# Performance work log

Hardware: AMD Instinct MI355X
Metric: run time of the kernel (lower is better)

Reference implementation:

```python
import jax, jax.numpy as jnp
import numpy as np

B, S, D = 2, 2048, 1024
HQ, HKV = 16, 4
HD = D // HQ          # 64
DKV = HKV * HD        # 256
G = HQ // HKV         # 4 kv groups
SCALE = HD ** -0.5


def setup_inputs() -> dict:
    key = jax.random.key(0)
    ks = jax.random.split(key, 9)
    s = 0.02
    return {
        "q": jax.random.normal(ks[0], (B, S, D), dtype=jnp.float32),
        "Wq": jax.random.normal(ks[1], (D, D), dtype=jnp.float32) * s,
        "bq": jnp.zeros((D,), dtype=jnp.float32),
        "Wk": jax.random.normal(ks[2], (D, DKV), dtype=jnp.float32) * s,
        "bk": jnp.zeros((DKV,), dtype=jnp.float32),
        "Wv": jax.random.normal(ks[3], (D, DKV), dtype=jnp.float32) * s,
        "bv": jnp.zeros((DKV,), dtype=jnp.float32),
        "Wo": jax.random.normal(ks[4], (D, D), dtype=jnp.float32) * s,
        "bo": jnp.zeros((D,), dtype=jnp.float32),
    }


def reference(q, Wq, bq, Wk, bk, Wv, bv, Wo, bo):
    # self-attention: k = v = q (module defaults)
    qp = q @ Wq + bq                       # [B,S,D]
    kp = q @ Wk + bk                       # [B,S,DKV]
    vp = q @ Wv + bv                       # [B,S,DKV]
    qh = qp.reshape(B, S, HQ, HD).transpose(0, 2, 1, 3)    # [B,HQ,S,HD]
    kh = kp.reshape(B, S, HKV, HD)
    vh = vp.reshape(B, S, HKV, HD)
    # repeat_interleave kv heads along head dim (each kv head serves G q-heads)
    kh = jnp.repeat(kh, G, axis=2).transpose(0, 2, 1, 3)   # [B,HQ,S,HD]
    vh = jnp.repeat(vh, G, axis=2).transpose(0, 2, 1, 3)   # [B,HQ,S,HD]
    scores = jnp.einsum("bhqd,bhkd->bhqk", qh, kh) * SCALE  # [B,HQ,S,S]
    attn = jax.nn.softmax(scores, axis=-1)
    out = jnp.einsum("bhqk,bhkd->bhqd", attn, vh)           # [B,HQ,S,HD]
    out = out.transpose(0, 2, 1, 3).reshape(B, S, D)
    out = out @ Wo + bo
    return out, attn
```

## Files before the change

kernel.cpp:

```cpp
#include <hip/hip_runtime.h>
#include <stdint.h>

#define B_ 2
#define S_ 2048
#define D_ 1024
#define HD_ 64
#define DKV_ 256

typedef __attribute__((ext_vector_type(8))) __bf16 bf16x8;
typedef __attribute__((ext_vector_type(4))) float f32x4;
typedef __attribute__((ext_vector_type(4))) float float4v;
typedef __attribute__((ext_vector_type(4))) short s16x4;

__device__ __forceinline__ unsigned short f2bf(float f) {
  union { float f; uint32_t u; } v; v.f = f;
  uint32_t r = v.u + 0x7FFFu + ((v.u >> 16) & 1u);
  return (unsigned short)(r >> 16);
}

__device__ __forceinline__ void gload16(const void* g, void* l) {
  __builtin_amdgcn_global_load_lds(
      (const __attribute__((address_space(1))) uint32_t*)g,
      (__attribute__((address_space(3))) uint32_t*)l, 16, 0, 0);
}

__device__ __forceinline__ f32x4 mfma16(bf16x8 a, bf16x8 b, f32x4 c) {
  return __builtin_amdgcn_mfma_f32_16x16x32_bf16(a, b, c, 0, 0, 0);
}

__global__ void k_cvt(const float* __restrict__ in, unsigned short* __restrict__ out) {
  size_t i = ((size_t)blockIdx.x * 256 + threadIdx.x) * 4;
  float4v f = *(const float4v*)(in + i);
  s16x4 o;
#pragma unroll
  for (int r = 0; r < 4; ++r) o[r] = (short)f2bf(f[r]);
  *(s16x4*)(out + i) = o;
}

__global__ void k_tcvt_all(const float* __restrict__ Wq, const float* __restrict__ Wk,
                           const float* __restrict__ Wv, const float* __restrict__ Wo,
                           unsigned short* __restrict__ WqT, unsigned short* __restrict__ WkT,
                           unsigned short* __restrict__ WvT, unsigned short* __restrict__ WoT) {
  __shared__ unsigned short t[32][33];
  const int x = blockIdx.x;
  const float* W;
  unsigned short* Wt;
  int N, n0;
  if (x < 32)      { W = Wq; Wt = WqT; N = 1024; n0 = x * 32; }
  else if (x < 40) { W = Wk; Wt = WkT; N = 256;  n0 = (x - 32) * 32; }
  else if (x < 48) { W = Wv; Wt = WvT; N = 256;  n0 = (x - 40) * 32; }
  else             { W = Wo; Wt = WoT; N = 1024; n0 = (x - 48) * 32; }
  const int K = 1024, k0 = blockIdx.y * 32;
  int tx = threadIdx.x & 31, ty = threadIdx.x >> 5;
#pragma unroll
  for (int i = 0; i < 32; i += 8)
    t[ty + i][tx] = f2bf(W[(size_t)(k0 + ty + i) * N + n0 + tx]);
  __syncthreads();
#pragma unroll
  for (int i = 0; i < 32; i += 8)
    Wt[(size_t)(n0 + ty + i) * K + k0 + tx] = t[tx][ty + i];
}

__global__ void k_tbf(const unsigned short* __restrict__ src, unsigned short* __restrict__ dst,
                      int R, int C) {
  __shared__ unsigned short t[32][33];
  size_t base = (size_t)blockIdx.z * R * C;
  int c0 = blockIdx.x * 32, r0 = blockIdx.y * 32;
  int tx = threadIdx.x & 31, ty = threadIdx.x >> 5;
#pragma unroll
  for (int i = 0; i < 32; i += 8)
    t[ty + i][tx] = src[base + (size_t)(r0 + ty + i) * C + c0 + tx];
  __syncthreads();
#pragma unroll
  for (int i = 0; i < 32; i += 8)
    dst[base + (size_t)(c0 + ty + i) * R + r0 + tx] = t[tx][ty + i];
}

template <bool OUTF32>
__device__ __forceinline__ void gemm_body64(
    const unsigned short* A, const unsigned short* Bt,
    const float* bias, void* Cout, int N, int K, int bx, int by) {
  __shared__ char lds[49152];
  const int lane = threadIdx.x & 63, wid = threadIdx.x >> 6;
  const int r15 = lane & 15, j = lane >> 4;
  const int wm = wid >> 1, wn = wid & 1;
  const size_t strideb = (size_t)K * 2;
  const char* Ab = (const char*)A + (size_t)bx * 128 * strideb;
  const char* Bb = (const char*)Bt + (size_t)by * 64 * strideb;
  const int srow = lane >> 3;
  const int scol = ((lane & 7) ^ srow) << 4;

  f32x4 acc[4][2];
#pragma unroll
  for (int a = 0; a < 4; ++a)
#pragma unroll
    for (int b = 0; b < 2; ++b) acc[a][b] = (f32x4){0.f, 0.f, 0.f, 0.f};

  auto stage = [&](int kt, int buf) {
    char* as = lds + buf * 24576;
    char* bs = as + 16384;
    const char* Ag = Ab + kt * 128;
    const char* Bg = Bb + kt * 128;
#pragma unroll
    for (int i = 0; i < 4; ++i) {
      int chunk = i * 4 + wid;
      gload16(Ag + (size_t)(chunk * 8 + srow) * strideb + scol, as + chunk * 1024);
    }
#pragma unroll
    for (int i = 0; i < 2; ++i) {
      int c2 = i * 4 + wid;
      gload16(Bg + (size_t)(c2 * 8 + srow) * strideb + scol, bs + c2 * 1024);
    }
  };

  stage(0, 0);
  __syncthreads();
  const int nk = K >> 6;
  const int ca0 = ((0 * 4 + j) ^ (r15 & 7)) << 4;
  const int ca1 = ((1 * 4 + j) ^ (r15 & 7)) << 4;

  for (int kt = 0; kt < nk; ++kt) {
    if (kt + 1 < nk) stage(kt + 1, (kt + 1) & 1);
    const char* as = lds + (kt & 1) * 24576;
    const char* bs = as + 16384;
    bf16x8 af[4][2], bfr[2][2];
#pragma unroll
    for (int mi = 0; mi < 4; ++mi) {
      int row = wm * 64 + mi * 16 + r15;
      af[mi][0] = *(const bf16x8*)(as + row * 128 + ca0);
      af[mi][1] = *(const bf16x8*)(as + row * 128 + ca1);
    }
#pragma unroll
    for (int ni = 0; ni < 2; ++ni) {
      int row = wn * 32 + ni * 16 + r15;
      bfr[ni][0] = *(const bf16x8*)(bs + row * 128 + ca0);
      bfr[ni][1] = *(const bf16x8*)(bs + row * 128 + ca1);
    }
#pragma unroll
    for (int kk = 0; kk < 2; ++kk)
#pragma unroll
      for (int mi = 0; mi < 4; ++mi)
#pragma unroll
        for (int ni = 0; ni < 2; ++ni)
          acc[mi][ni] = mfma16(af[mi][kk], bfr[ni][kk], acc[mi][ni]);
    __syncthreads();
  }

#pragma unroll
  for (int ni = 0; ni < 2; ++ni) {
    int col = by * 64 + wn * 32 + ni * 16 + r15;
    float bv = bias[col];
#pragma unroll
    for (int mi = 0; mi < 4; ++mi) {
      int row0 = bx * 128 + wm * 64 + mi * 16 + j * 4;
#pragma unroll
      for (int r = 0; r < 4; ++r) {
        float v = acc[mi][ni][r] + bv;
        if (OUTF32)
          ((float*)Cout)[(size_t)(row0 + r) * N + col] = v;
        else
          ((unsigned short*)Cout)[(size_t)(row0 + r) * N + col] = f2bf(v);
      }
    }
  }
}

__global__ __launch_bounds__(256, 3) void k_gemm_qkv(
    const unsigned short* __restrict__ A,
    const unsigned short* __restrict__ WqT, const unsigned short* __restrict__ WkT,
    const unsigned short* __restrict__ WvT,
    const float* __restrict__ bq, const float* __restrict__ bk, const float* __restrict__ bv,
    unsigned short* __restrict__ qpB, unsigned short* __restrict__ kpB,
    unsigned short* __restrict__ vpB) {
  int y = blockIdx.y;
  const unsigned short* Bt;
  const float* bias;
  unsigned short* out;
  int N, ycol;
  if (y < 16)     { Bt = WqT; bias = bq; out = qpB; N = 1024; ycol = y; }
  else if (y < 20){ Bt = WkT; bias = bk; out = kpB; N = 256;  ycol = y - 16; }
  else            { Bt = WvT; bias = bv; out = vpB; N = 256;  ycol = y - 20; }
  gemm_body64<false>(A, Bt, bias, out, N, 1024, blockIdx.x, ycol);
}

__global__ __launch_bounds__(256, 3) void k_gemm_o(
    const unsigned short* __restrict__ A, const unsigned short* __restrict__ Bt,
    const float* __restrict__ bias, float* __restrict__ Cout) {
  gemm_body64<true>(A, Bt, bias, Cout, 1024, 1024, blockIdx.x, blockIdx.y);
}

__global__ __launch_bounds__(256, 4) void k_attn(
    const unsigned short* __restrict__ qp, const unsigned short* __restrict__ kp,
    const unsigned short* __restrict__ vpT, float* __restrict__ attn,
    unsigned short* __restrict__ ctx) {
  __shared__ char lds[40960];
  char* Ks = lds;
  char* VTs = lds + 16384;
  char* Ps = lds + 32768;

  const int lane = threadIdx.x & 63, wid = threadIdx.x >> 6;
  const int r15 = lane & 15, j = lane >> 4;
  const int srow = lane >> 3;
  const int scol = ((lane & 7) ^ srow) << 4;

  const int lid = blockIdx.x;
  const int grp = lid & 7, inner = lid >> 3;
  const int h2 = inner >> 5, qt = inner & 31;
  const int b = grp >> 2, kv = grp & 3, h = kv * 4 + h2;
  const int bh = b * 16 + h;
  const int q0 = qt * 64 + wid * 16;

  const char* kbase = (const char*)kp + ((size_t)(b * S_) * DKV_ + kv * HD_) * 2;
  const char* vtb = (const char*)vpT + ((size_t)(b * DKV_ + kv * HD_)) * S_ * 2;
  float* attnb = attn + ((size_t)bh * S_ + q0) * S_;
  char* psw = Ps + wid * 2048;

  auto stageK = [&](int kt, int buf) {
#pragma unroll
    for (int i = 0; i < 2; ++i)
      gload16(kbase + (size_t)(kt * 64 + wid * 16 + i * 8 + srow) * (DKV_ * 2) + scol,
              Ks + buf * 8192 + wid * 2048 + i * 1024);
  };
  auto stageVT = [&](int kt, int buf) {
#pragma unroll
    for (int i = 0; i < 2; ++i)
      gload16(vtb + (size_t)(wid * 16 + i * 8 + srow) * (S_ * 2) + kt * 128 + scol,
              VTs + buf * 8192 + wid * 2048 + i * 1024);
  };

  const char* qr = (const char*)qp + ((size_t)(b * S_ + q0 + r15) * D_ + h * HD_) * 2;
  const bf16x8 bq0 = *(const bf16x8*)(qr + j * 16);
  const bf16x8 bq1 = *(const bf16x8*)(qr + 64 + j * 16);

  const float cs = 0.125f * 1.44269504088896f;

  auto qk = [&](const char* ks, f32x4 (&z)[4]) {
#pragma unroll
    for (int f = 0; f < 4; ++f) {
      int krow = f * 16 + r15;
      bf16x8 a0 = *(const bf16x8*)(ks + krow * 128 + ((j ^ (krow & 7)) << 4));
      bf16x8 a1 = *(const bf16x8*)(ks + krow * 128 + (((4 + j) ^ (krow & 7)) << 4));
      f32x4 t = mfma16(a0, bq0, (f32x4){0.f, 0.f, 0.f, 0.f});
      z[f] = mfma16(a1, bq1, t);
    }
  };

  float lsum = 0.f;
  stageK(0, 0);
  asm volatile("s_waitcnt vmcnt(0)" ::: "memory");
  __syncthreads();
#pragma unroll 1
  for (int kt = 0; kt < 32; ++kt) {
    const int cur = kt & 1;
    if (kt + 1 < 32) stageK(kt + 1, cur ^ 1);
    f32x4 z[4];
    qk(Ks + cur * 8192, z);
#pragma unroll
    for (int f = 0; f < 4; ++f) {
      f32x4 p;
#pragma unroll
      for (int r = 0; r < 4; ++r) p[r] = exp2f(z[f][r] * cs);
      lsum += (p[0] + p[1]) + (p[2] + p[3]);
    }
    asm volatile("s_waitcnt vmcnt(0)" ::: "memory");
    __syncthreads();
  }

  lsum += __shfl_xor(lsum, 16, 64);
  lsum += __shfl_xor(lsum, 32, 64);
  const float invl = 1.f / lsum;

  f32x4 o[4];
#pragma unroll
  for (int nf = 0; nf < 4; ++nf) o[nf] = (f32x4){0.f, 0.f, 0.f, 0.f};

  stageK(0, 0);
  stageVT(0, 0);
  asm volatile("s_waitcnt vmcnt(0)" ::: "memory");
  __syncthreads();
#pragma unroll 1
  for (int kt = 0; kt < 32; ++kt) {
    const int cur = kt & 1;
    if (kt + 1 < 32) { stageK(kt + 1, cur ^ 1); stageVT(kt + 1, cur ^ 1); }
    f32x4 z[4];
    qk(Ks + cur * 8192, z);
#pragma unroll
    for (int f = 0; f < 4; ++f) {
      float4v pv;
#pragma unroll
      for (int r = 0; r < 4; ++r) pv[r] = exp2f(z[f][r] * cs) * invl;
      *(float4v*)(attnb + (size_t)r15 * S_ + kt * 64 + f * 16 + j * 4) = pv;
      s16x4 pb;
#pragma unroll
      for (int r = 0; r < 4; ++r) pb[r] = (short)f2bf(pv[r]);
      *(s16x4*)(psw + r15 * 128 +
                ((((f * 2 + (j >> 1)) ^ (r15 & 7)) << 4) | ((j & 1) * 8))) = pb;
    }
    const char* vs = VTs + cur * 8192;
#pragma unroll
    for (int ks2 = 0; ks2 < 2; ++ks2) {
      bf16x8 pa = *(const bf16x8*)(psw + r15 * 128 + (((ks2 * 4 + j) ^ (r15 & 7)) << 4));
#pragma unroll
      for (int nf = 0; nf < 4; ++nf) {
        int vrow = nf * 16 + r15;
        bf16x8 vb = *(const bf16x8*)(vs + vrow * 128 + (((ks2 * 4 + j) ^ (vrow & 7)) << 4));
        o[nf] = mfma16(pa, vb, o[nf]);
      }
    }
    asm volatile("s_waitcnt vmcnt(0)" ::: "memory");
    __syncthreads();
  }

#pragma unroll
  for (int nf = 0; nf < 4; ++nf)
#pragma unroll
    for (int r = 0; r < 4; ++r)
      ctx[((size_t)(b * S_ + q0 + j * 4 + r)) * D_ + h * HD_ + nf * 16 + r15] =
          f2bf(o[nf][r]);
}

extern "C" void kernel_launch(void* const* d_in, const int* in_sizes, int n_in,
                              void* d_out, int out_size, void* d_ws, size_t ws_size,
                              hipStream_t stream) {
  (void)in_sizes; (void)n_in; (void)out_size; (void)ws_size;
  const float* q = (const float*)d_in[0];
  const float* Wq = (const float*)d_in[1];
  const float* bq = (const float*)d_in[2];
  const float* Wk = (const float*)d_in[3];
  const float* bk = (const float*)d_in[4];
  const float* Wv = (const float*)d_in[5];
  const float* bv = (const float*)d_in[6];
  const float* Wo = (const float*)d_in[7];
  const float* bo = (const float*)d_in[8];

  char* ws = (char*)d_ws;
  unsigned short* qbf = (unsigned short*)(ws);
  unsigned short* qpB = (unsigned short*)(ws + (8u << 20));
  unsigned short* kpB = (unsigned short*)(ws + (16u << 20));
  unsigned short* vpB = (unsigned short*)(ws + (18u << 20));
  unsigned short* vpT = (unsigned short*)(ws + (20u << 20));
  unsigned short* ctx = (unsigned short*)(ws + (22u << 20));
  unsigned short* WqT = (unsigned short*)(ws + (30u << 20));
  unsigned short* WkT = (unsigned short*)(ws + (32u << 20));
  unsigned short* WvT = (unsigned short*)(ws + (32u << 20) + (512u << 10));
  unsigned short* WoT = (unsigned short*)(ws + (33u << 20));

  float* out = (float*)d_out;
  float* attn = out + (size_t)B_ * S_ * D_;

  k_cvt<<<4096, 256, 0, stream>>>(q, qbf);
  k_tcvt_all<<<dim3(80, 32), 256, 0, stream>>>(Wq, Wk, Wv, Wo, WqT, WkT, WvT, WoT);

  k_gemm_qkv<<<dim3(32, 24), 256, 0, stream>>>(qbf, WqT, WkT, WvT, bq, bk, bv,
                                               qpB, kpB, vpB);
  k_tbf<<<dim3(8, 64, 2), 256, 0, stream>>>(vpB, vpT, 2048, 256);

  k_attn<<<1024, 256, 0, stream>>>(qpB, kpB, vpT, attn, ctx);

  k_gemm_o<<<dim3(32, 16), 256, 0, stream>>>(ctx, WoT, bo, out);
}
```

Baseline: 203.4 us.

## Fuse input conversion kernels, write V transposed from GEMM epilogue, relax attention wait

The q conversion and weight transpose-convert kernels are merged into one launch using extra grid blocks. The QKV GEMM now writes V directly in transposed [b][col][s] layout from its epilogue, which removes the separate transpose kernel and its intermediate buffer. The attention loop's end-of-iteration wait is relaxed from vmcnt(0) to vmcnt(4) with a raw barrier, so some outstanding prefetch loads can stay in flight. This cuts two launches and one memory round trip, but the partial wait risks reading data before it has landed if the load count is wrong.

```diff
diff --git a/kernel.cpp b/kernel.cpp
--- a/kernel.cpp
+++ b/kernel.cpp
@@ -28,21 +28,22 @@
   return __builtin_amdgcn_mfma_f32_16x16x32_bf16(a, b, c, 0, 0, 0);
 }
 
-__global__ void k_cvt(const float* __restrict__ in, unsigned short* __restrict__ out) {
-  size_t i = ((size_t)blockIdx.x * 256 + threadIdx.x) * 4;
-  float4v f = *(const float4v*)(in + i);
-  s16x4 o;
-#pragma unroll
-  for (int r = 0; r < 4; ++r) o[r] = (short)f2bf(f[r]);
-  *(s16x4*)(out + i) = o;
-}
-
-__global__ void k_tcvt_all(const float* __restrict__ Wq, const float* __restrict__ Wk,
-                           const float* __restrict__ Wv, const float* __restrict__ Wo,
-                           unsigned short* __restrict__ WqT, unsigned short* __restrict__ WkT,
-                           unsigned short* __restrict__ WvT, unsigned short* __restrict__ WoT) {
+__global__ void k_prep(const float* __restrict__ q, unsigned short* __restrict__ qbf,
+                       const float* __restrict__ Wq, const float* __restrict__ Wk,
+                       const float* __restrict__ Wv, const float* __restrict__ Wo,
+                       unsigned short* __restrict__ WqT, unsigned short* __restrict__ WkT,
+                       unsigned short* __restrict__ WvT, unsigned short* __restrict__ WoT) {
+  const int x = blockIdx.x;
+  if (x >= 80) {
+    size_t i = (((size_t)(x - 80) * 32 + blockIdx.y) * 256 + threadIdx.x) * 4;
+    float4v f = *(const float4v*)(q + i);
+    s16x4 o;
+#pragma unroll
+    for (int r = 0; r < 4; ++r) o[r] = (short)f2bf(f[r]);
+    *(s16x4*)(qbf + i) = o;
+    return;
+  }
   __shared__ unsigned short t[32][33];
-  const int x = blockIdx.x;
   const float* W;
   unsigned short* Wt;
   int N, n0;
@@ -61,22 +62,7 @@
     Wt[(size_t)(n0 + ty + i) * K + k0 + tx] = t[tx][ty + i];
 }
 
-__global__ void k_tbf(const unsigned short* __restrict__ src, unsigned short* __restrict__ dst,
-                      int R, int C) {
-  __shared__ unsigned short t[32][33];
-  size_t base = (size_t)blockIdx.z * R * C;
-  int c0 = blockIdx.x * 32, r0 = blockIdx.y * 32;
-  int tx = threadIdx.x & 31, ty = threadIdx.x >> 5;
-#pragma unroll
-  for (int i = 0; i < 32; i += 8)
-    t[ty + i][tx] = src[base + (size_t)(r0 + ty + i) * C + c0 + tx];
-  __syncthreads();
-#pragma unroll
-  for (int i = 0; i < 32; i += 8)
-    dst[base + (size_t)(c0 + ty + i) * R + r0 + tx] = t[tx][ty + i];
-}
-
-template <bool OUTF32>
+template <int MODE>
 __device__ __forceinline__ void gemm_body64(
     const unsigned short* A, const unsigned short* Bt,
     const float* bias, void* Cout, int N, int K, int bx, int by) {
@@ -153,13 +139,21 @@
 #pragma unroll
     for (int mi = 0; mi < 4; ++mi) {
       int row0 = bx * 128 + wm * 64 + mi * 16 + j * 4;
-#pragma unroll
-      for (int r = 0; r < 4; ++r) {
-        float v = acc[mi][ni][r] + bv;
-        if (OUTF32)
-          ((float*)Cout)[(size_t)(row0 + r) * N + col] = v;
-        else
-          ((unsigned short*)Cout)[(size_t)(row0 + r) * N + col] = f2bf(v);
+      if (MODE == 2) {
+        s16x4 pb;
+#pragma unroll
+        for (int r = 0; r < 4; ++r) pb[r] = (short)f2bf(acc[mi][ni][r] + bv);
+        size_t base = ((size_t)((row0 >> 11) * DKV_ + col)) * S_ + (row0 & 2047);
+        *(s16x4*)((unsigned short*)Cout + base) = pb;
+      } else {
+#pragma unroll
+        for (int r = 0; r < 4; ++r) {
+          float v = acc[mi][ni][r] + bv;
+          if (MODE == 1)
+            ((float*)Cout)[(size_t)(row0 + r) * N + col] = v;
+          else
+            ((unsigned short*)Cout)[(size_t)(row0 + r) * N + col] = f2bf(v);
+        }
       }
     }
   }
@@ -171,22 +165,20 @@
     const unsigned short* __restrict__ WvT,
     const float* __restrict__ bq, const float* __restrict__ bk, const float* __restrict__ bv,
     unsigned short* __restrict__ qpB, unsigned short* __restrict__ kpB,
-    unsigned short* __restrict__ vpB) {
+    unsigned short* __restrict__ vpT) {
   int y = blockIdx.y;
-  const unsigned short* Bt;
-  const float* bias;
-  unsigned short* out;
-  int N, ycol;
-  if (y < 16)     { Bt = WqT; bias = bq; out = qpB; N = 1024; ycol = y; }
-  else if (y < 20){ Bt = WkT; bias = bk; out = kpB; N = 256;  ycol = y - 16; }
-  else            { Bt = WvT; bias = bv; out = vpB; N = 256;  ycol = y - 20; }
-  gemm_body64<false>(A, Bt, bias, out, N, 1024, blockIdx.x, ycol);
+  if (y < 16)
+    gemm_body64<0>(A, WqT, bq, qpB, 1024, 1024, blockIdx.x, y);
+  else if (y < 20)
+    gemm_body64<0>(A, WkT, bk, kpB, 256, 1024, blockIdx.x, y - 16);
+  else
+    gemm_body64<2>(A, WvT, bv, vpT, 256, 1024, blockIdx.x, y - 20);
 }
 
 __global__ __launch_bounds__(256, 3) void k_gemm_o(
     const unsigned short* __restrict__ A, const unsigned short* __restrict__ Bt,
     const float* __restrict__ bias, float* __restrict__ Cout) {
-  gemm_body64<true>(A, Bt, bias, Cout, 1024, 1024, blockIdx.x, blockIdx.y);
+  gemm_body64<1>(A, Bt, bias, Cout, 1024, 1024, blockIdx.x, blockIdx.y);
 }
 
 __global__ __launch_bounds__(256, 4) void k_attn(
@@ -307,8 +299,8 @@
         o[nf] = mfma16(pa, vb, o[nf]);
       }
     }
-    asm volatile("s_waitcnt vmcnt(0)" ::: "memory");
-    __syncthreads();
+    asm volatile("s_waitcnt vmcnt(4)" ::: "memory");
+    __builtin_amdgcn_s_barrier();
   }
 
 #pragma unroll
@@ -337,7 +329,6 @@
   unsigned short* qbf = (unsigned short*)(ws);
   unsigned short* qpB = (unsigned short*)(ws + (8u << 20));
   unsigned short* kpB = (unsigned short*)(ws + (16u << 20));
-  unsigned short* vpB = (unsigned short*)(ws + (18u << 20));
   unsigned short* vpT = (unsigned short*)(ws + (20u << 20));
   unsigned short* ctx = (unsigned short*)(ws + (22u << 20));
   unsigned short* WqT = (unsigned short*)(ws + (30u << 20));
@@ -348,12 +339,11 @@
   float* out = (float*)d_out;
   float* attn = out + (size_t)B_ * S_ * D_;
 
-  k_cvt<<<4096, 256, 0, stream>>>(q, qbf);
-  k_tcvt_all<<<dim3(80, 32), 256, 0, stream>>>(Wq, Wk, Wv, Wo, WqT, WkT, WvT, WoT);
+  k_prep<<<dim3(208, 32), 256, 0, stream>>>(q, qbf, Wq, Wk, Wv, Wo,
+                                            WqT, WkT, WvT, WoT);
 
   k_gemm_qkv<<<dim3(32, 24), 256, 0, stream>>>(qbf, WqT, WkT, WvT, bq, bk, bv,
-                                               qpB, kpB, vpB);
-  k_tbf<<<dim3(8, 64, 2), 256, 0, stream>>>(vpB, vpT, 2048, 256);
+                                               qpB, kpB, vpT);
 
   k_attn<<<1024, 256, 0, stream>>>(qpB, kpB, vpT, attn, ctx);
 
```

Result: slower. 208.9 us (+2.7%).
